# Performance work log

Measured on AMD Instinct MI355X. Metric: run time of the kernel, lower is better.

Reference implementation:

```python
import jax, jax.numpy as jnp
import numpy as np

B, S, D = 2, 2048, 2048
H, G = 32, 8           # num_heads, num_groups
HD = D // H            # head_dim = 64
GS = H // G            # group_size = 4


def setup_inputs() -> dict:
    key = jax.random.key(0)
    ks = jax.random.split(key, 11)
    s = 0.02
    return {
        "x": jax.random.normal(ks[0], (B, S, D), dtype=jnp.float32),
        "kv": jax.random.normal(ks[1], (B, S, D), dtype=jnp.float32),
        "Wq": jax.random.normal(ks[2], (D, D), dtype=jnp.float32) * s,
        "bq": jnp.zeros((D,), dtype=jnp.float32),
        "Wk": jax.random.normal(ks[3], (D, G * HD), dtype=jnp.float32) * s,
        "bk": jnp.zeros((G * HD,), dtype=jnp.float32),
        "Wv": jax.random.normal(ks[4], (D, G * HD), dtype=jnp.float32) * s,
        "bv": jnp.zeros((G * HD,), dtype=jnp.float32),
        "Wo": jax.random.normal(ks[5], (D, D), dtype=jnp.float32) * s,
        "bo": jnp.zeros((D,), dtype=jnp.float32),
        "expanding_context": 0,
    }


def reference(x, kv, Wq, bq, Wk, bk, Wv, bv, Wo, bo, expanding_context):
    # expanding_context is ignored when use_kv_cache=False (matches torch module)
    b, s, d = x.shape
    q = (x @ Wq + bq).reshape(b, s, H, HD).transpose(0, 2, 1, 3)      # [B,H,S,HD]
    k = (kv @ Wk + bk).reshape(b, s, G, HD).transpose(0, 2, 1, 3)     # [B,G,S,HD]
    v = (kv @ Wv + bv).reshape(b, s, G, HD).transpose(0, 2, 1, 3)     # [B,G,S,HD]
    # repeat_interleave KV heads to match query heads
    k = jnp.repeat(k, GS, axis=1)                                      # [B,H,S,HD]
    v = jnp.repeat(v, GS, axis=1)
    scale = 1.0 / jnp.sqrt(jnp.array(HD, dtype=x.dtype))
    scores = jnp.einsum("bhqd,bhkd->bhqk", q, k) * scale              # [B,H,S,S]
    causal = jnp.tril(jnp.ones((s, s), dtype=bool))                    # True where allowed
    scores = jnp.where(causal[None, None], scores, jnp.finfo(x.dtype).min)
    attn = jax.nn.softmax(scores, axis=-1)
    out = jnp.einsum("bhqk,bhkd->bhqd", attn, v)                      # [B,H,S,HD]
    out = out.transpose(0, 2, 1, 3).reshape(b, s, D)                  # [B,S,D]
    return out @ Wo + bo
```

## Files before the change

### kernel.cpp

```cpp
#include <hip/hip_runtime.h>
#include <hip/hip_bf16.h>
#include <stdint.h>

namespace {
constexpr int CB = 2, CS = 2048, CD = 2048, CH = 32, CG = 8, CHD = 64, CGS = 4;

typedef __bf16 bf16x8 __attribute__((ext_vector_type(8)));
typedef float f32x4 __attribute__((ext_vector_type(4)));
typedef float f32x16 __attribute__((ext_vector_type(16)));
typedef uint32_t u32x4 __attribute__((ext_vector_type(4)));

__device__ inline uint16_t f2bf(float f) {
  uint32_t u = __float_as_uint(f);
  u += 0x7fffu + ((u >> 16) & 1u);
  return (uint16_t)(u >> 16);
}

__device__ inline void gload_lds16(const void* g, void* l) {
  __builtin_amdgcn_global_load_lds(
      (const __attribute__((address_space(1))) void*)g,
      (__attribute__((address_space(3))) void*)l, 16, 0, 0);
}

__device__ inline uint32_t cvtpk_bf16(float lo, float hi) {
  uint32_t r;
  asm("v_cvt_pk_bf16_f32 %0, %1, %2" : "=v"(r) : "v"(lo), "v"(hi));
  return r;
}
__device__ inline void pl32swap(uint32_t& a, uint32_t& b) {
  asm("v_permlane32_swap_b32 %0, %1" : "+v"(a), "+v"(b));
}
}

__global__ __launch_bounds__(256) void cast_both_kernel(
    const float* __restrict__ x, const float* __restrict__ kv,
    uint16_t* __restrict__ xb, uint16_t* __restrict__ kvb, int nel) {
  int i = (blockIdx.x * 256 + threadIdx.x) * 4;
  const float* in;
  uint16_t* out;
  if (i < nel) { in = x + i; out = xb + i; }
  else         { in = kv + (i - nel); out = kvb + (i - nel); }
  const float4 v = *(const float4*)in;
  ushort4 o;
  o.x = f2bf(v.x); o.y = f2bf(v.y); o.z = f2bf(v.z); o.w = f2bf(v.w);
  *(ushort4*)out = o;
}

__global__ __launch_bounds__(256) void transpose_all_kernel(
    const float* __restrict__ Wq, const float* __restrict__ Wk,
    const float* __restrict__ Wv, const float* __restrict__ Wo,
    uint16_t* __restrict__ out) {
  __shared__ uint16_t tile[32][33];
  const int gn0 = blockIdx.x * 32;
  const int k0 = blockIdx.y * 32;
  const float* in;
  int Nr, start;
  if (gn0 < 2048)      { in = Wq; Nr = 2048; start = 0; }
  else if (gn0 < 2560) { in = Wk; Nr = 512;  start = 2048; }
  else if (gn0 < 3072) { in = Wv; Nr = 512;  start = 2560; }
  else                 { in = Wo; Nr = 2048; start = 3072; }
  const int n0 = gn0 - start;
  const int tx = threadIdx.x & 31, tg = threadIdx.x >> 5;
#pragma unroll
  for (int rr = 0; rr < 4; ++rr) {
    int k = tg * 4 + rr;
    tile[k][tx] = f2bf(in[(size_t)(k0 + k) * Nr + n0 + tx]);
  }
  __syncthreads();
#pragma unroll
  for (int rr = 0; rr < 4; ++rr) {
    int n = tg * 4 + rr;
    out[(size_t)(gn0 + n) * CD + k0 + tx] = tile[tx][n];
  }
}

__global__ __launch_bounds__(256, 2) void gemm_qkv_kernel(
    const uint16_t* __restrict__ xb, const uint16_t* __restrict__ kvb,
    const uint16_t* __restrict__ WT,
    const float* __restrict__ bq, const float* __restrict__ bk,
    const float* __restrict__ bv,
    uint16_t* __restrict__ Qb, uint16_t* __restrict__ Kb,
    uint16_t* __restrict__ VTb) {
  constexpr int BM = 128, BN = 128, BK = 32, K = 2048, NT = K / BK;
  constexpr int ASZ = BM * BK;
  constexpr int BSZ = BN * BK;
  constexpr int BUFSZ = ASZ + BSZ;
  __shared__ uint16_t smem[3 * BUFSZ];
  const int tid = threadIdx.x;
  const int w = tid >> 6, l = tid & 63;
  const int wr = w >> 1, wc = w & 1;
  const int l15 = l & 15, lq = l >> 4;

  const int gx = gridDim.x;
  int bid = blockIdx.y * gx + blockIdx.x;
  const int nwg = gx * gridDim.y;
  bid = (bid & 7) * (nwg >> 3) + (bid >> 3);
  const int m0 = (bid / gx) * BM, n0 = (bid % gx) * BN;
  const uint16_t* A = (n0 < 2048) ? xb : kvb;

  auto stage = [&](int buf, int kt) {
    uint16_t* base = smem + buf * BUFSZ;
    const int k0 = kt * BK;
#pragma unroll
    for (int i = 0; i < 2; ++i) {
      int g = i * 256 + tid;
      int row = g >> 2, slot = g & 3;
      int kq = slot ^ ((row >> 1) & 3);
      gload_lds16(A + (size_t)(m0 + row) * K + k0 + kq * 8, base + g * 8);
    }
#pragma unroll
    for (int i = 0; i < 2; ++i) {
      int g = i * 256 + tid;
      int row = g >> 2, slot = g & 3;
      int kq = slot ^ ((row >> 1) & 3);
      gload_lds16(WT + (size_t)(n0 + row) * K + k0 + kq * 8,
                  base + ASZ + g * 8);
    }
  };

  int aOff[4], bOff[4];
#pragma unroll
  for (int m = 0; m < 4; ++m) {
    int row = wr * 64 + m * 16 + l15;
    aOff[m] = (row * BK + (lq ^ ((row >> 1) & 3)) * 8) * 2;
  }
#pragma unroll
  for (int n = 0; n < 4; ++n) {
    int row = wc * 64 + n * 16 + l15;
    bOff[n] = ASZ * 2 + (row * BK + (lq ^ ((row >> 1) & 3)) * 8) * 2;
  }

  f32x4 acc[4][4] = {};

  stage(0, 0);
  stage(1, 1);

  int bt = 0, bs = 2;
  for (int t = 0; t < NT; ++t) {
    if (t < NT - 1) asm volatile("s_waitcnt vmcnt(4)" ::: "memory");
    else            asm volatile("s_waitcnt vmcnt(0)" ::: "memory");
    __builtin_amdgcn_s_barrier();
    asm volatile("" ::: "memory");

    const char* buf = (const char*)(smem + bt * BUFSZ);
    bf16x8 af[4], bfr[4];
#pragma unroll
    for (int m = 0; m < 4; ++m) af[m] = *(const bf16x8*)(buf + aOff[m]);
#pragma unroll
    for (int n = 0; n < 4; ++n) bfr[n] = *(const bf16x8*)(buf + bOff[n]);

    if (t + 2 < NT) stage(bs, t + 2);

    __builtin_amdgcn_s_setprio(1);
#pragma unroll
    for (int m = 0; m < 4; ++m)
#pragma unroll
      for (int n = 0; n < 4; ++n)
        acc[m][n] = __builtin_amdgcn_mfma_f32_16x16x32_bf16(
            af[m], bfr[n], acc[m][n], 0, 0, 0);
    __builtin_amdgcn_s_setprio(0);

    bt = bt == 2 ? 0 : bt + 1;
    bs = bs == 2 ? 0 : bs + 1;
  }

#pragma unroll
  for (int m = 0; m < 4; ++m)
#pragma unroll
    for (int n = 0; n < 4; ++n)
#pragma unroll
      for (int r = 0; r < 4; ++r) {
        int gm = m0 + wr * 64 + m * 16 + lq * 4 + r;
        int gn = n0 + wc * 64 + n * 16 + l15;
        int b = gm >> 11, s = gm & (CS - 1);
        if (n0 < 2048) {
          float v = (acc[m][n][r] + bq[gn]) * (0.125f * 1.44269504088896340736f);
          int h = gn >> 6, hd = gn & 63;
          Qb[(((size_t)(b * CH + h)) * CS + s) * CHD + hd] = f2bf(v);
        } else if (n0 < 2560) {
          int gn2 = gn - 2048;
          float v = acc[m][n][r] + bk[gn2];
          int gh = gn2 >> 6, hd = gn2 & 63;
          Kb[(((size_t)(b * CG + gh)) * CS + s) * CHD + hd] = f2bf(v);
        } else {
          int gn2 = gn - 2560;
          float v = acc[m][n][r] + bv[gn2];
          int gh = gn2 >> 6, hd = gn2 & 63;
          VTb[(((size_t)(b * CG + gh)) * CHD + hd) * CS + s] = f2bf(v);
        }
      }
}

__global__ __launch_bounds__(256, 2) void gemm_out_kernel(
    const uint16_t* __restrict__ A, const uint16_t* __restrict__ Bt,
    const float* __restrict__ bias, float* __restrict__ Cout,
    int M, int N, int Kdim) {
  constexpr int BM = 128, BN = 128, BK = 32, K = 2048, NT = K / BK;
  constexpr int ASZ = BM * BK;
  constexpr int BSZ = BN * BK;
  constexpr int BUFSZ = ASZ + BSZ;
  __shared__ uint16_t smem[3 * BUFSZ];
  const int tid = threadIdx.x;
  const int w = tid >> 6, l = tid & 63;
  const int wr = w >> 1, wc = w & 1;
  const int l15 = l & 15, lq = l >> 4;

  const int gx = gridDim.x;
  int bid = blockIdx.y * gx + blockIdx.x;
  const int nwg = gx * gridDim.y;
  bid = (bid & 7) * (nwg >> 3) + (bid >> 3);
  const int m0 = (bid / gx) * BM, n0 = (bid % gx) * BN;

  auto stage = [&](int buf, int kt) {
    uint16_t* base = smem + buf * BUFSZ;
    const int k0 = kt * BK;
#pragma unroll
    for (int i = 0; i < 2; ++i) {
      int g = i * 256 + tid;
      int row = g >> 2, slot = g & 3;
      int kq = slot ^ ((row >> 1) & 3);
      gload_lds16(A + (size_t)(m0 + row) * K + k0 + kq * 8, base + g * 8);
    }
#pragma unroll
    for (int i = 0; i < 2; ++i) {
      int g = i * 256 + tid;
      int row = g >> 2, slot = g & 3;
      int kq = slot ^ ((row >> 1) & 3);
      gload_lds16(Bt + (size_t)(n0 + row) * K + k0 + kq * 8,
                  base + ASZ + g * 8);
    }
  };

  int aOff[4], bOff[4];
#pragma unroll
  for (int m = 0; m < 4; ++m) {
    int row = wr * 64 + m * 16 + l15;
    aOff[m] = (row * BK + (lq ^ ((row >> 1) & 3)) * 8) * 2;
  }
#pragma unroll
  for (int n = 0; n < 4; ++n) {
    int row = wc * 64 + n * 16 + l15;
    bOff[n] = ASZ * 2 + (row * BK + (lq ^ ((row >> 1) & 3)) * 8) * 2;
  }

  f32x4 acc[4][4] = {};

  stage(0, 0);
  stage(1, 1);

  int bt = 0, bs = 2;
  for (int t = 0; t < NT; ++t) {
    if (t < NT - 1) asm volatile("s_waitcnt vmcnt(4)" ::: "memory");
    else            asm volatile("s_waitcnt vmcnt(0)" ::: "memory");
    __builtin_amdgcn_s_barrier();
    asm volatile("" ::: "memory");

    const char* buf = (const char*)(smem + bt * BUFSZ);
    bf16x8 af[4], bfr[4];
#pragma unroll
    for (int m = 0; m < 4; ++m) af[m] = *(const bf16x8*)(buf + aOff[m]);
#pragma unroll
    for (int n = 0; n < 4; ++n) bfr[n] = *(const bf16x8*)(buf + bOff[n]);

    if (t + 2 < NT) stage(bs, t + 2);

    __builtin_amdgcn_s_setprio(1);
#pragma unroll
    for (int m = 0; m < 4; ++m)
#pragma unroll
      for (int n = 0; n < 4; ++n)
        acc[m][n] = __builtin_amdgcn_mfma_f32_16x16x32_bf16(
            af[m], bfr[n], acc[m][n], 0, 0, 0);
    __builtin_amdgcn_s_setprio(0);

    bt = bt == 2 ? 0 : bt + 1;
    bs = bs == 2 ? 0 : bs + 1;
  }

#pragma unroll
  for (int m = 0; m < 4; ++m)
#pragma unroll
    for (int n = 0; n < 4; ++n)
#pragma unroll
      for (int r = 0; r < 4; ++r) {
        int gm = m0 + wr * 64 + m * 16 + lq * 4 + r;
        int gn = n0 + wc * 64 + n * 16 + l15;
        Cout[(size_t)gm * N + gn] = acc[m][n][r] + bias[gn];
      }
}

__global__ __launch_bounds__(256, 2) void flash_attn_kernel(
    const uint16_t* __restrict__ Q, const uint16_t* __restrict__ K,
    const uint16_t* __restrict__ VT, uint16_t* __restrict__ Aout) {
  constexpr int NQB = CS / 128;
  constexpr int KV = 128;
  __shared__ __align__(16) uint16_t Ksm[2][KV * CHD];
  __shared__ __align__(16) uint16_t Vsm[2][CHD * KV];
  const int tid = threadIdx.x, w = tid >> 6, l = tid & 63;
  const int l31 = l & 31, hi = l >> 5;
  const int x = blockIdx.x;
  const int h = blockIdx.y, b = blockIdx.z, g = h >> 2;

  const uint16_t* Qbase = Q + ((size_t)(b * CH + h)) * CS * CHD;
  const uint16_t* Kbase = K + ((size_t)(b * CG + g)) * CS * CHD;
  const uint16_t* Vbase = VT + ((size_t)(b * CG + g)) * CHD * CS;

  auto stage = [&](int buf, int kt) {
#pragma unroll
    for (int i = 0; i < 4; ++i) {
      int gK = i * 256 + tid;
      int rowK = gK >> 3, slotK = gK & 7;
      int kqK = slotK ^ (rowK & 7);
      gload_lds16(Kbase + ((size_t)kt * KV + rowK) * CHD + kqK * 8,
                  &Ksm[buf][gK * 8]);
    }
#pragma unroll
    for (int i = 0; i < 4; ++i) {
      int gV = i * 256 + tid;
      int rowV = gV >> 4, slotV = gV & 15;
      int kqV = slotV ^ (rowV & 15);
      gload_lds16(Vbase + (size_t)rowV * CS + kt * KV + kqV * 8,
                  &Vsm[buf][gV * 8]);
    }
  };

  int kOff[4][4];
#pragma unroll
  for (int c = 0; c < 4; ++c)
#pragma unroll
    for (int kc = 0; kc < 4; ++kc) {
      int row = c * 32 + l31;
      kOff[c][kc] = ((row * CHD + kc * 16 + hi * 8) * 2) ^ ((row & 7) << 4);
    }
  int vOff[2][8];
#pragma unroll
  for (int c = 0; c < 2; ++c)
#pragma unroll
    for (int ks = 0; ks < 8; ++ks) {
      int row = c * 32 + l31;
      vOff[c][ks] = ((row * KV + ks * 16 + hi * 8) * 2) ^ ((row & 15) << 4);
    }

#pragma unroll 1
  for (int job = 0; job < 2; ++job) {
    const int qb = job == 0 ? (NQB - 1 - x) : x;
    const int qrow = qb * 128 + w * 32 + l31;
    const int wbase = qb * 128 + w * 32;

    bf16x8 qf[4];
#pragma unroll
    for (int kc = 0; kc < 4; ++kc)
      qf[kc] = *(const bf16x8*)(Qbase + (size_t)qrow * CHD + kc * 16 + hi * 8);

    f32x16 o0 = {}, o1 = {};
    float mrun = -3e38f, lrun = 0.f;
    const int nt = qb + 1;

    stage(0, 0);
    asm volatile("s_waitcnt vmcnt(0)" ::: "memory");
    __syncthreads();

    for (int kt = 0; kt < nt; ++kt) {
      const int cur = kt & 1;
      if (kt + 1 < nt) stage(cur ^ 1, kt + 1);

      const char* ksmb = (const char*)Ksm[cur];
      const char* vsmb = (const char*)Vsm[cur];

      f32x16 p0 = {}, p1 = {}, p2 = {}, p3 = {};
      __builtin_amdgcn_s_setprio(1);
#pragma unroll
      for (int kc = 0; kc < 4; ++kc) {
        bf16x8 ka0 = *(const bf16x8*)(ksmb + kOff[0][kc]);
        bf16x8 ka1 = *(const bf16x8*)(ksmb + kOff[1][kc]);
        bf16x8 ka2 = *(const bf16x8*)(ksmb + kOff[2][kc]);
        bf16x8 ka3 = *(const bf16x8*)(ksmb + kOff[3][kc]);
        p0 = __builtin_amdgcn_mfma_f32_32x32x16_bf16(ka0, qf[kc], p0, 0, 0, 0);
        p1 = __builtin_amdgcn_mfma_f32_32x32x16_bf16(ka1, qf[kc], p1, 0, 0, 0);
        p2 = __builtin_amdgcn_mfma_f32_32x32x16_bf16(ka2, qf[kc], p2, 0, 0, 0);
        p3 = __builtin_amdgcn_mfma_f32_32x32x16_bf16(ka3, qf[kc], p3, 0, 0, 0);
      }
      __builtin_amdgcn_s_setprio(0);

      const bool need_mask = (kt * KV + KV - 1 > wbase);
      if (need_mask) {
#pragma unroll
        for (int r = 0; r < 16; ++r) {
          int keyb = kt * KV + (r & 3) + 8 * (r >> 2) + 4 * hi;
          if (keyb > qrow) p0[r] = -3e38f;
          if (keyb + 32 > qrow) p1[r] = -3e38f;
          if (keyb + 64 > qrow) p2[r] = -3e38f;
          if (keyb + 96 > qrow) p3[r] = -3e38f;
        }
      }
      float pmax = -3e38f;
#pragma unroll
      for (int r = 0; r < 16; ++r) {
        pmax = fmaxf(pmax, fmaxf(fmaxf(p0[r], p1[r]), fmaxf(p2[r], p3[r])));
      }
      pmax = fmaxf(pmax, __shfl_xor(pmax, 32));

      if (!__all(pmax <= mrun + 8.f)) {
        float mnew = fmaxf(mrun, pmax);
        float alpha = __builtin_amdgcn_exp2f(mrun - mnew);
#pragma unroll
        for (int r = 0; r < 16; ++r) { o0[r] *= alpha; o1[r] *= alpha; }
        lrun *= alpha;
        mrun = mnew;
      }
      float s = 0.f;
#pragma unroll
      for (int r = 0; r < 16; ++r) {
        float e0 = __builtin_amdgcn_exp2f(p0[r] - mrun);
        float e1 = __builtin_amdgcn_exp2f(p1[r] - mrun);
        float e2 = __builtin_amdgcn_exp2f(p2[r] - mrun);
        float e3 = __builtin_amdgcn_exp2f(p3[r] - mrun);
        p0[r] = e0; p1[r] = e1; p2[r] = e2; p3[r] = e3;
        s += (e0 + e1) + (e2 + e3);
      }
      s += __shfl_xor(s, 32);
      lrun += s;

      u32x4 paw[8];
#pragma unroll
      for (int k = 0; k < 8; ++k) {
        const int base = (k & 1) * 8;
        const int c = k >> 1;
        const f32x16& pc = (c == 0) ? p0 : (c == 1) ? p1 : (c == 2) ? p2 : p3;
        uint32_t c01 = cvtpk_bf16(pc[base + 0], pc[base + 1]);
        uint32_t c23 = cvtpk_bf16(pc[base + 2], pc[base + 3]);
        uint32_t c45 = cvtpk_bf16(pc[base + 4], pc[base + 5]);
        uint32_t c67 = cvtpk_bf16(pc[base + 6], pc[base + 7]);
        pl32swap(c01, c45);
        pl32swap(c23, c67);
        paw[k] = (u32x4){c01, c23, c45, c67};
      }

      __builtin_amdgcn_s_setprio(1);
#pragma unroll
      for (int ks = 0; ks < 8; ++ks) {
        bf16x8 vb0 = *(const bf16x8*)(vsmb + vOff[0][ks]);
        bf16x8 vb1 = *(const bf16x8*)(vsmb + vOff[1][ks]);
        bf16x8 pb = __builtin_bit_cast(bf16x8, paw[ks]);
        o0 = __builtin_amdgcn_mfma_f32_32x32x16_bf16(vb0, pb, o0, 0, 0, 0);
        o1 = __builtin_amdgcn_mfma_f32_32x32x16_bf16(vb1, pb, o1, 0, 0, 0);
      }
      __builtin_amdgcn_s_setprio(0);

      asm volatile("s_waitcnt vmcnt(0)" ::: "memory");
      __syncthreads();
    }

    float invl = 1.f / lrun;
    uint16_t* orow = Aout + ((size_t)b * CS + qrow) * CD + (size_t)h * CHD;
#pragma unroll
    for (int k = 0; k < 8; ++k) {
      int reg = 2 * k;
      int hd = (reg & 3) + 8 * (reg >> 2) + 4 * hi;
      *(uint32_t*)(orow + hd) = cvtpk_bf16(o0[reg] * invl, o0[reg + 1] * invl);
      *(uint32_t*)(orow + hd + 32) = cvtpk_bf16(o1[reg] * invl, o1[reg + 1] * invl);
    }
  }
}

extern "C" void kernel_launch(void* const* d_in, const int* in_sizes, int n_in,
                              void* d_out, int out_size, void* d_ws, size_t ws_size,
                              hipStream_t stream) {
  const float* x = (const float*)d_in[0];
  const float* kv = (const float*)d_in[1];
  const float* Wq = (const float*)d_in[2];
  const float* bq = (const float*)d_in[3];
  const float* Wk = (const float*)d_in[4];
  const float* bk = (const float*)d_in[5];
  const float* Wv = (const float*)d_in[6];
  const float* bv = (const float*)d_in[7];
  const float* Wo = (const float*)d_in[8];
  const float* bo = (const float*)d_in[9];
  float* out = (float*)d_out;

  char* ws = (char*)d_ws;
  uint16_t* xb = (uint16_t*)ws;   ws += (size_t)CB * CS * CD * 2;
  uint16_t* kvb = (uint16_t*)ws;  ws += (size_t)CB * CS * CD * 2;
  uint16_t* WqT = (uint16_t*)ws;  ws += (size_t)CD * CD * 2;
  uint16_t* WkT = (uint16_t*)ws;  ws += (size_t)(CG * CHD) * CD * 2;
  uint16_t* WvT = (uint16_t*)ws;  ws += (size_t)(CG * CHD) * CD * 2;
  uint16_t* WoT = (uint16_t*)ws;  ws += (size_t)CD * CD * 2;
  uint16_t* Qb = (uint16_t*)ws;   ws += (size_t)CB * CH * CS * CHD * 2;
  uint16_t* Kb = (uint16_t*)ws;   ws += (size_t)CB * CG * CS * CHD * 2;
  uint16_t* VTb = (uint16_t*)ws;  ws += (size_t)CB * CG * CHD * CS * 2;
  uint16_t* attnb = (uint16_t*)ws;
  (void)WkT; (void)WvT;

  const int NTOK = CB * CS;
  const int nel = CB * CS * CD;

  cast_both_kernel<<<2 * nel / 4 / 256, 256, 0, stream>>>(x, kv, xb, kvb, nel);
  transpose_all_kernel<<<dim3(5120 / 32, CD / 32), 256, 0, stream>>>(
      Wq, Wk, Wv, Wo, WqT);

  gemm_qkv_kernel<<<dim3(3072 / 128, NTOK / 128), 256, 0, stream>>>(
      xb, kvb, WqT, bq, bk, bv, Qb, Kb, VTb);

  flash_attn_kernel<<<dim3(CS / 256, CH, CB), 256, 0, stream>>>(Qb, Kb, VTb, attnb);

  gemm_out_kernel<<<dim3(CD / 128, NTOK / 128), 256, 0, stream>>>(
      attnb, WoT, bo, out, NTOK, CD, CD);
}
```

Before: 200.7 us.

## Pre-pack weights in MFMA fragment order and load B directly to registers

The weight transpose kernel now writes bf16 weights in a fragment-packed layout, 16-row by 32-k blocks with each lane's 8 values contiguous. Both GEMM kernels then load B operands straight from global memory into registers with one coalesced 16-byte load per lane. They stage only A through LDS, using double-buffered B registers and an unrolled even/odd loop. This removes B's LDS traffic and LDS space and is meant to cut LDS bandwidth and capacity pressure. In exchange it relies on direct global-load latency being hidden by the two-step prefetch, adds register pressure, and drops the LDS reuse of B across waves that share a column.

```diff
diff --git a/kernel.cpp b/kernel.cpp
--- a/kernel.cpp
+++ b/kernel.cpp
@@ -9,6 +9,7 @@
 typedef float f32x4 __attribute__((ext_vector_type(4)));
 typedef float f32x16 __attribute__((ext_vector_type(16)));
 typedef uint32_t u32x4 __attribute__((ext_vector_type(4)));
+typedef uint16_t u16x8 __attribute__((ext_vector_type(8)));
 
 __device__ inline uint16_t f2bf(float f) {
   uint32_t u = __float_as_uint(f);
@@ -67,25 +68,28 @@
     tile[k][tx] = f2bf(in[(size_t)(k0 + k) * Nr + n0 + tx]);
   }
   __syncthreads();
-#pragma unroll
-  for (int rr = 0; rr < 4; ++rr) {
-    int n = tg * 4 + rr;
-    out[(size_t)(gn0 + n) * CD + k0 + tx] = tile[tx][n];
+  if (threadIdx.x < 128) {
+    int n = threadIdx.x >> 2, k8 = threadIdx.x & 3;
+    u16x8 v;
+#pragma unroll
+    for (int j = 0; j < 8; ++j) v[j] = tile[k8 * 8 + j][n];
+    int n_abs = gn0 + n;
+    size_t flat = (((size_t)(n_abs >> 4) * 64 + (size_t)(k0 >> 5)) * 64 +
+                   (size_t)(k8 * 16 + (n_abs & 15))) * 8;
+    *(u16x8*)(out + flat) = v;
   }
 }
 
 __global__ __launch_bounds__(256, 2) void gemm_qkv_kernel(
     const uint16_t* __restrict__ xb, const uint16_t* __restrict__ kvb,
-    const uint16_t* __restrict__ WT,
+    const uint16_t* __restrict__ WTp,
     const float* __restrict__ bq, const float* __restrict__ bk,
     const float* __restrict__ bv,
     uint16_t* __restrict__ Qb, uint16_t* __restrict__ Kb,
     uint16_t* __restrict__ VTb) {
-  constexpr int BM = 128, BN = 128, BK = 32, K = 2048, NT = K / BK;
+  constexpr int BM = 128, BK = 32, K = 2048, NT = K / BK;
   constexpr int ASZ = BM * BK;
-  constexpr int BSZ = BN * BK;
-  constexpr int BUFSZ = ASZ + BSZ;
-  __shared__ uint16_t smem[3 * BUFSZ];
+  __shared__ uint16_t Asm[3 * ASZ];
   const int tid = threadIdx.x;
   const int w = tid >> 6, l = tid & 63;
   const int wr = w >> 1, wc = w & 1;
@@ -95,12 +99,13 @@
   int bid = blockIdx.y * gx + blockIdx.x;
   const int nwg = gx * gridDim.y;
   bid = (bid & 7) * (nwg >> 3) + (bid >> 3);
-  const int m0 = (bid / gx) * BM, n0 = (bid % gx) * BN;
+  const int m0 = (bid / gx) * BM, n0 = (bid % gx) * 128;
   const uint16_t* A = (n0 < 2048) ? xb : kvb;
-
-  auto stage = [&](int buf, int kt) {
-    uint16_t* base = smem + buf * BUFSZ;
-    const int k0 = kt * BK;
+  const int nbb = (n0 >> 4) + wc * 4;
+
+  auto stageA = [&](int buf, int t) {
+    uint16_t* base = Asm + buf * ASZ;
+    const int k0 = t * BK;
 #pragma unroll
     for (int i = 0; i < 2; ++i) {
       int g = i * 256 + tid;
@@ -108,61 +113,56 @@
       int kq = slot ^ ((row >> 1) & 3);
       gload_lds16(A + (size_t)(m0 + row) * K + k0 + kq * 8, base + g * 8);
     }
-#pragma unroll
-    for (int i = 0; i < 2; ++i) {
-      int g = i * 256 + tid;
-      int row = g >> 2, slot = g & 3;
-      int kq = slot ^ ((row >> 1) & 3);
-      gload_lds16(WT + (size_t)(n0 + row) * K + k0 + kq * 8,
-                  base + ASZ + g * 8);
-    }
   };
-
-  int aOff[4], bOff[4];
+  auto loadB = [&](bf16x8* dst, int t) {
+#pragma unroll
+    for (int n = 0; n < 4; ++n)
+      dst[n] = *(const bf16x8*)(
+          WTp + ((((size_t)(nbb + n)) * 64 + (size_t)t) << 9) + (size_t)l * 8);
+  };
+
+  int aOff[4];
 #pragma unroll
   for (int m = 0; m < 4; ++m) {
     int row = wr * 64 + m * 16 + l15;
     aOff[m] = (row * BK + (lq ^ ((row >> 1) & 3)) * 8) * 2;
   }
-#pragma unroll
-  for (int n = 0; n < 4; ++n) {
-    int row = wc * 64 + n * 16 + l15;
-    bOff[n] = ASZ * 2 + (row * BK + (lq ^ ((row >> 1) & 3)) * 8) * 2;
-  }
 
   f32x4 acc[4][4] = {};
-
-  stage(0, 0);
-  stage(1, 1);
+  bf16x8 bE[4], bO[4];
+
+  loadB(bE, 0); stageA(0, 0);
+  loadB(bO, 1); stageA(1, 1);
 
   int bt = 0, bs = 2;
-  for (int t = 0; t < NT; ++t) {
-    if (t < NT - 1) asm volatile("s_waitcnt vmcnt(4)" ::: "memory");
-    else            asm volatile("s_waitcnt vmcnt(0)" ::: "memory");
-    __builtin_amdgcn_s_barrier();
-    asm volatile("" ::: "memory");
-
-    const char* buf = (const char*)(smem + bt * BUFSZ);
-    bf16x8 af[4], bfr[4];
-#pragma unroll
-    for (int m = 0; m < 4; ++m) af[m] = *(const bf16x8*)(buf + aOff[m]);
-#pragma unroll
-    for (int n = 0; n < 4; ++n) bfr[n] = *(const bf16x8*)(buf + bOff[n]);
-
-    if (t + 2 < NT) stage(bs, t + 2);
-
-    __builtin_amdgcn_s_setprio(1);
-#pragma unroll
-    for (int m = 0; m < 4; ++m)
-#pragma unroll
-      for (int n = 0; n < 4; ++n)
-        acc[m][n] = __builtin_amdgcn_mfma_f32_16x16x32_bf16(
-            af[m], bfr[n], acc[m][n], 0, 0, 0);
-    __builtin_amdgcn_s_setprio(0);
-
-    bt = bt == 2 ? 0 : bt + 1;
-    bs = bs == 2 ? 0 : bs + 1;
-  }
+
+#define QKV_SUB(T, BREG, VM)                                                 \
+  {                                                                          \
+    asm volatile("s_waitcnt vmcnt(" #VM ")" ::: "memory");                   \
+    __builtin_amdgcn_s_barrier();                                            \
+    asm volatile("" ::: "memory");                                           \
+    const char* buf_ = (const char*)(Asm + bt * ASZ);                        \
+    bf16x8 af[4];                                                            \
+    _Pragma("unroll") for (int m = 0; m < 4; ++m)                            \
+        af[m] = *(const bf16x8*)(buf_ + aOff[m]);                            \
+    __builtin_amdgcn_s_setprio(1);                                           \
+    _Pragma("unroll") for (int m = 0; m < 4; ++m)                            \
+        _Pragma("unroll") for (int n = 0; n < 4; ++n)                        \
+            acc[m][n] = __builtin_amdgcn_mfma_f32_16x16x32_bf16(             \
+                af[m], BREG[n], acc[m][n], 0, 0, 0);                         \
+    __builtin_amdgcn_s_setprio(0);                                           \
+    if ((T) + 2 < NT) { loadB(BREG, (T) + 2); stageA(bs, (T) + 2); }         \
+    bt = bt == 2 ? 0 : bt + 1;                                               \
+    bs = bs == 2 ? 0 : bs + 1;                                               \
+  }
+
+  for (int t = 0; t < NT - 2; t += 2) {
+    QKV_SUB(t, bE, 6);
+    QKV_SUB(t + 1, bO, 6);
+  }
+  QKV_SUB(NT - 2, bE, 6);
+  QKV_SUB(NT - 1, bO, 0);
+#undef QKV_SUB
 
 #pragma unroll
   for (int m = 0; m < 4; ++m)
@@ -192,14 +192,12 @@
 }
 
 __global__ __launch_bounds__(256, 2) void gemm_out_kernel(
-    const uint16_t* __restrict__ A, const uint16_t* __restrict__ Bt,
+    const uint16_t* __restrict__ A, const uint16_t* __restrict__ Btp,
     const float* __restrict__ bias, float* __restrict__ Cout,
     int M, int N, int Kdim) {
-  constexpr int BM = 128, BN = 128, BK = 32, K = 2048, NT = K / BK;
+  constexpr int BM = 128, BK = 32, K = 2048, NT = K / BK;
   constexpr int ASZ = BM * BK;
-  constexpr int BSZ = BN * BK;
-  constexpr int BUFSZ = ASZ + BSZ;
-  __shared__ uint16_t smem[3 * BUFSZ];
+  __shared__ uint16_t Asm[3 * ASZ];
   const int tid = threadIdx.x;
   const int w = tid >> 6, l = tid & 63;
   const int wr = w >> 1, wc = w & 1;
@@ -209,11 +207,12 @@
   int bid = blockIdx.y * gx + blockIdx.x;
   const int nwg = gx * gridDim.y;
   bid = (bid & 7) * (nwg >> 3) + (bid >> 3);
-  const int m0 = (bid / gx) * BM, n0 = (bid % gx) * BN;
-
-  auto stage = [&](int buf, int kt) {
-    uint16_t* base = smem + buf * BUFSZ;
-    const int k0 = kt * BK;
+  const int m0 = (bid / gx) * BM, n0 = (bid % gx) * 128;
+  const int nbb = (n0 >> 4) + wc * 4;
+
+  auto stageA = [&](int buf, int t) {
+    uint16_t* base = Asm + buf * ASZ;
+    const int k0 = t * BK;
 #pragma unroll
     for (int i = 0; i < 2; ++i) {
       int g = i * 256 + tid;
@@ -221,61 +220,56 @@
       int kq = slot ^ ((row >> 1) & 3);
       gload_lds16(A + (size_t)(m0 + row) * K + k0 + kq * 8, base + g * 8);
     }
-#pragma unroll
-    for (int i = 0; i < 2; ++i) {
-      int g = i * 256 + tid;
-      int row = g >> 2, slot = g & 3;
-      int kq = slot ^ ((row >> 1) & 3);
-      gload_lds16(Bt + (size_t)(n0 + row) * K + k0 + kq * 8,
-                  base + ASZ + g * 8);
-    }
   };
-
-  int aOff[4], bOff[4];
+  auto loadB = [&](bf16x8* dst, int t) {
+#pragma unroll
+    for (int n = 0; n < 4; ++n)
+      dst[n] = *(const bf16x8*)(
+          Btp + ((((size_t)(nbb + n)) * 64 + (size_t)t) << 9) + (size_t)l * 8);
+  };
+
+  int aOff[4];
 #pragma unroll
   for (int m = 0; m < 4; ++m) {
     int row = wr * 64 + m * 16 + l15;
     aOff[m] = (row * BK + (lq ^ ((row >> 1) & 3)) * 8) * 2;
   }
-#pragma unroll
-  for (int n = 0; n < 4; ++n) {
-    int row = wc * 64 + n * 16 + l15;
-    bOff[n] = ASZ * 2 + (row * BK + (lq ^ ((row >> 1) & 3)) * 8) * 2;
-  }
 
   f32x4 acc[4][4] = {};
-
-  stage(0, 0);
-  stage(1, 1);
+  bf16x8 bE[4], bO[4];
+
+  loadB(bE, 0); stageA(0, 0);
+  loadB(bO, 1); stageA(1, 1);
 
   int bt = 0, bs = 2;
-  for (int t = 0; t < NT; ++t) {
-    if (t < NT - 1) asm volatile("s_waitcnt vmcnt(4)" ::: "memory");
-    else            asm volatile("s_waitcnt vmcnt(0)" ::: "memory");
-    __builtin_amdgcn_s_barrier();
-    asm volatile("" ::: "memory");
-
-    const char* buf = (const char*)(smem + bt * BUFSZ);
-    bf16x8 af[4], bfr[4];
-#pragma unroll
-    for (int m = 0; m < 4; ++m) af[m] = *(const bf16x8*)(buf + aOff[m]);
-#pragma unroll
-    for (int n = 0; n < 4; ++n) bfr[n] = *(const bf16x8*)(buf + bOff[n]);
-
-    if (t + 2 < NT) stage(bs, t + 2);
-
-    __builtin_amdgcn_s_setprio(1);
-#pragma unroll
-    for (int m = 0; m < 4; ++m)
-#pragma unroll
-      for (int n = 0; n < 4; ++n)
-        acc[m][n] = __builtin_amdgcn_mfma_f32_16x16x32_bf16(
-            af[m], bfr[n], acc[m][n], 0, 0, 0);
-    __builtin_amdgcn_s_setprio(0);
-
-    bt = bt == 2 ? 0 : bt + 1;
-    bs = bs == 2 ? 0 : bs + 1;
-  }
+
+#define OUT_SUB(T, BREG, VM)                                                 \
+  {                                                                          \
+    asm volatile("s_waitcnt vmcnt(" #VM ")" ::: "memory");                   \
+    __builtin_amdgcn_s_barrier();                                            \
+    asm volatile("" ::: "memory");                                           \
+    const char* buf_ = (const char*)(Asm + bt * ASZ);                        \
+    bf16x8 af[4];                                                            \
+    _Pragma("unroll") for (int m = 0; m < 4; ++m)                            \
+        af[m] = *(const bf16x8*)(buf_ + aOff[m]);                            \
+    __builtin_amdgcn_s_setprio(1);                                           \
+    _Pragma("unroll") for (int m = 0; m < 4; ++m)                            \
+        _Pragma("unroll") for (int n = 0; n < 4; ++n)                        \
+            acc[m][n] = __builtin_amdgcn_mfma_f32_16x16x32_bf16(             \
+                af[m], BREG[n], acc[m][n], 0, 0, 0);                         \
+    __builtin_amdgcn_s_setprio(0);                                           \
+    if ((T) + 2 < NT) { loadB(BREG, (T) + 2); stageA(bs, (T) + 2); }         \
+    bt = bt == 2 ? 0 : bt + 1;                                               \
+    bs = bs == 2 ? 0 : bs + 1;                                               \
+  }
+
+  for (int t = 0; t < NT - 2; t += 2) {
+    OUT_SUB(t, bE, 6);
+    OUT_SUB(t + 1, bO, 6);
+  }
+  OUT_SUB(NT - 2, bE, 6);
+  OUT_SUB(NT - 1, bO, 0);
+#undef OUT_SUB
 
 #pragma unroll
   for (int m = 0; m < 4; ++m)
```

After: 195.6 us. 1.03x faster.

## Pre-pack weights into MFMA fragment layout and load B directly to registers

Applied to the files above, without the earlier changes.

The weight-transpose kernel now writes weights in a fragment-packed layout, so each wave can load its B operand for an MFMA straight from global memory into registers with one contiguous 16-byte load per lane. The two GEMM kernels therefore stage only A through LDS, and BK doubles to 64, which halves the number of barrier-separated iterations. Occupancy is raised to 3 blocks per SM via launch bounds. The aim is to cut LDS traffic and per-iteration overhead. The cost is that B loads become global-latency register prefetches with only one iteration of lead time, and register pressure goes up.

```diff
diff --git a/kernel.cpp b/kernel.cpp
--- a/kernel.cpp
+++ b/kernel.cpp
@@ -9,6 +9,7 @@
 typedef float f32x4 __attribute__((ext_vector_type(4)));
 typedef float f32x16 __attribute__((ext_vector_type(16)));
 typedef uint32_t u32x4 __attribute__((ext_vector_type(4)));
+typedef uint16_t u16x8 __attribute__((ext_vector_type(8)));
 
 __device__ inline uint16_t f2bf(float f) {
   uint32_t u = __float_as_uint(f);
@@ -67,25 +68,28 @@
     tile[k][tx] = f2bf(in[(size_t)(k0 + k) * Nr + n0 + tx]);
   }
   __syncthreads();
-#pragma unroll
-  for (int rr = 0; rr < 4; ++rr) {
-    int n = tg * 4 + rr;
-    out[(size_t)(gn0 + n) * CD + k0 + tx] = tile[tx][n];
+  if (threadIdx.x < 128) {
+    int n = threadIdx.x >> 2, k8 = threadIdx.x & 3;
+    u16x8 v;
+#pragma unroll
+    for (int j = 0; j < 8; ++j) v[j] = tile[k8 * 8 + j][n];
+    int n_abs = gn0 + n;
+    size_t flat = (((size_t)(n_abs >> 4) * 64 + (size_t)(k0 >> 5)) * 64 +
+                   (size_t)(k8 * 16 + (n_abs & 15))) * 8;
+    *(u16x8*)(out + flat) = v;
   }
 }
 
-__global__ __launch_bounds__(256, 2) void gemm_qkv_kernel(
+__global__ __launch_bounds__(256, 3) void gemm_qkv_kernel(
     const uint16_t* __restrict__ xb, const uint16_t* __restrict__ kvb,
-    const uint16_t* __restrict__ WT,
+    const uint16_t* __restrict__ WTp,
     const float* __restrict__ bq, const float* __restrict__ bk,
     const float* __restrict__ bv,
     uint16_t* __restrict__ Qb, uint16_t* __restrict__ Kb,
     uint16_t* __restrict__ VTb) {
-  constexpr int BM = 128, BN = 128, BK = 32, K = 2048, NT = K / BK;
+  constexpr int BM = 128, BK = 64, K = 2048, NT = K / BK;
   constexpr int ASZ = BM * BK;
-  constexpr int BSZ = BN * BK;
-  constexpr int BUFSZ = ASZ + BSZ;
-  __shared__ uint16_t smem[3 * BUFSZ];
+  __shared__ uint16_t Asm[3 * ASZ];
   const int tid = threadIdx.x;
   const int w = tid >> 6, l = tid & 63;
   const int wr = w >> 1, wc = w & 1;
@@ -95,45 +99,46 @@
   int bid = blockIdx.y * gx + blockIdx.x;
   const int nwg = gx * gridDim.y;
   bid = (bid & 7) * (nwg >> 3) + (bid >> 3);
-  const int m0 = (bid / gx) * BM, n0 = (bid % gx) * BN;
+  const int m0 = (bid / gx) * BM, n0 = (bid % gx) * 128;
   const uint16_t* A = (n0 < 2048) ? xb : kvb;
-
-  auto stage = [&](int buf, int kt) {
-    uint16_t* base = smem + buf * BUFSZ;
-    const int k0 = kt * BK;
-#pragma unroll
-    for (int i = 0; i < 2; ++i) {
+  const int nbb = (n0 >> 4) + wc * 4;
+
+  auto stageA = [&](int buf, int t) {
+    uint16_t* base = Asm + buf * ASZ;
+    const int k0 = t * BK;
+#pragma unroll
+    for (int i = 0; i < 4; ++i) {
       int g = i * 256 + tid;
-      int row = g >> 2, slot = g & 3;
-      int kq = slot ^ ((row >> 1) & 3);
+      int row = g >> 3, slot = g & 7;
+      int kq = slot ^ (row & 7);
       gload_lds16(A + (size_t)(m0 + row) * K + k0 + kq * 8, base + g * 8);
     }
-#pragma unroll
-    for (int i = 0; i < 2; ++i) {
-      int g = i * 256 + tid;
-      int row = g >> 2, slot = g & 3;
-      int kq = slot ^ ((row >> 1) & 3);
-      gload_lds16(WT + (size_t)(n0 + row) * K + k0 + kq * 8,
-                  base + ASZ + g * 8);
-    }
   };
-
-  int aOff[4], bOff[4];
-#pragma unroll
-  for (int m = 0; m < 4; ++m) {
-    int row = wr * 64 + m * 16 + l15;
-    aOff[m] = (row * BK + (lq ^ ((row >> 1) & 3)) * 8) * 2;
-  }
-#pragma unroll
-  for (int n = 0; n < 4; ++n) {
-    int row = wc * 64 + n * 16 + l15;
-    bOff[n] = ASZ * 2 + (row * BK + (lq ^ ((row >> 1) & 3)) * 8) * 2;
-  }
+  auto loadB = [&](bf16x8 (*dst)[4], int t) {
+#pragma unroll
+    for (int kk = 0; kk < 2; ++kk)
+#pragma unroll
+      for (int n = 0; n < 4; ++n)
+        dst[kk][n] = *(const bf16x8*)(
+            WTp + ((((size_t)(nbb + n)) * 64 + (size_t)(2 * t + kk)) << 9) +
+            (size_t)l * 8);
+  };
+
+  int aOff[2][4];
+#pragma unroll
+  for (int kk = 0; kk < 2; ++kk)
+#pragma unroll
+    for (int m = 0; m < 4; ++m) {
+      int row = wr * 64 + m * 16 + l15;
+      aOff[kk][m] = (row * BK + ((kk * 4 + lq) ^ (row & 7)) * 8) * 2;
+    }
 
   f32x4 acc[4][4] = {};
-
-  stage(0, 0);
-  stage(1, 1);
+  bf16x8 brg[2][4];
+
+  loadB(brg, 0);
+  stageA(0, 0);
+  stageA(1, 1);
 
   int bt = 0, bs = 2;
   for (int t = 0; t < NT; ++t) {
@@ -142,23 +147,27 @@
     __builtin_amdgcn_s_barrier();
     asm volatile("" ::: "memory");
 
-    const char* buf = (const char*)(smem + bt * BUFSZ);
-    bf16x8 af[4], bfr[4];
-#pragma unroll
-    for (int m = 0; m < 4; ++m) af[m] = *(const bf16x8*)(buf + aOff[m]);
-#pragma unroll
-    for (int n = 0; n < 4; ++n) bfr[n] = *(const bf16x8*)(buf + bOff[n]);
-
-    if (t + 2 < NT) stage(bs, t + 2);
+    const char* buf = (const char*)(Asm + bt * ASZ);
+    bf16x8 af[2][4];
+#pragma unroll
+    for (int kk = 0; kk < 2; ++kk)
+#pragma unroll
+      for (int m = 0; m < 4; ++m)
+        af[kk][m] = *(const bf16x8*)(buf + aOff[kk][m]);
 
     __builtin_amdgcn_s_setprio(1);
 #pragma unroll
-    for (int m = 0; m < 4; ++m)
-#pragma unroll
-      for (int n = 0; n < 4; ++n)
-        acc[m][n] = __builtin_amdgcn_mfma_f32_16x16x32_bf16(
-            af[m], bfr[n], acc[m][n], 0, 0, 0);
+    for (int kk = 0; kk < 2; ++kk)
+#pragma unroll
+      for (int m = 0; m < 4; ++m)
+#pragma unroll
+        for (int n = 0; n < 4; ++n)
+          acc[m][n] = __builtin_amdgcn_mfma_f32_16x16x32_bf16(
+              af[kk][m], brg[kk][n], acc[m][n], 0, 0, 0);
     __builtin_amdgcn_s_setprio(0);
+
+    if (t + 1 < NT) loadB(brg, t + 1);
+    if (t + 2 < NT) stageA(bs, t + 2);
 
     bt = bt == 2 ? 0 : bt + 1;
     bs = bs == 2 ? 0 : bs + 1;
@@ -191,15 +200,13 @@
       }
 }
 
-__global__ __launch_bounds__(256, 2) void gemm_out_kernel(
-    const uint16_t* __restrict__ A, const uint16_t* __restrict__ Bt,
+__global__ __launch_bounds__(256, 3) void gemm_out_kernel(
+    const uint16_t* __restrict__ A, const uint16_t* __restrict__ Btp,
     const float* __restrict__ bias, float* __restrict__ Cout,
     int M, int N, int Kdim) {
-  constexpr int BM = 128, BN = 128, BK = 32, K = 2048, NT = K / BK;
+  constexpr int BM = 128, BK = 64, K = 2048, NT = K / BK;
   constexpr int ASZ = BM * BK;
-  constexpr int BSZ = BN * BK;
-  constexpr int BUFSZ = ASZ + BSZ;
-  __shared__ uint16_t smem[3 * BUFSZ];
+  __shared__ uint16_t Asm[3 * ASZ];
   const int tid = threadIdx.x;
   const int w = tid >> 6, l = tid & 63;
   const int wr = w >> 1, wc = w & 1;
@@ -209,44 +216,45 @@
   int bid = blockIdx.y * gx + blockIdx.x;
   const int nwg = gx * gridDim.y;
   bid = (bid & 7) * (nwg >> 3) + (bid >> 3);
-  const int m0 = (bid / gx) * BM, n0 = (bid % gx) * BN;
-
-  auto stage = [&](int buf, int kt) {
-    uint16_t* base = smem + buf * BUFSZ;
-    const int k0 = kt * BK;
-#pragma unroll
-    for (int i = 0; i < 2; ++i) {
+  const int m0 = (bid / gx) * BM, n0 = (bid % gx) * 128;
+  const int nbb = (n0 >> 4) + wc * 4;
+
+  auto stageA = [&](int buf, int t) {
+    uint16_t* base = Asm + buf * ASZ;
+    const int k0 = t * BK;
+#pragma unroll
+    for (int i = 0; i < 4; ++i) {
       int g = i * 256 + tid;
-      int row = g >> 2, slot = g & 3;
-      int kq = slot ^ ((row >> 1) & 3);
+      int row = g >> 3, slot = g & 7;
+      int kq = slot ^ (row & 7);
       gload_lds16(A + (size_t)(m0 + row) * K + k0 + kq * 8, base + g * 8);
     }
-#pragma unroll
-    for (int i = 0; i < 2; ++i) {
-      int g = i * 256 + tid;
-      int row = g >> 2, slot = g & 3;
-      int kq = slot ^ ((row >> 1) & 3);
-      gload_lds16(Bt + (size_t)(n0 + row) * K + k0 + kq * 8,
-                  base + ASZ + g * 8);
-    }
   };
-
-  int aOff[4], bOff[4];
-#pragma unroll
-  for (int m = 0; m < 4; ++m) {
-    int row = wr * 64 + m * 16 + l15;
-    aOff[m] = (row * BK + (lq ^ ((row >> 1) & 3)) * 8) * 2;
-  }
-#pragma unroll
-  for (int n = 0; n < 4; ++n) {
-    int row = wc * 64 + n * 16 + l15;
-    bOff[n] = ASZ * 2 + (row * BK + (lq ^ ((row >> 1) & 3)) * 8) * 2;
-  }
+  auto loadB = [&](bf16x8 (*dst)[4], int t) {
+#pragma unroll
+    for (int kk = 0; kk < 2; ++kk)
+#pragma unroll
+      for (int n = 0; n < 4; ++n)
+        dst[kk][n] = *(const bf16x8*)(
+            Btp + ((((size_t)(nbb + n)) * 64 + (size_t)(2 * t + kk)) << 9) +
+            (size_t)l * 8);
+  };
+
+  int aOff[2][4];
+#pragma unroll
+  for (int kk = 0; kk < 2; ++kk)
+#pragma unroll
+    for (int m = 0; m < 4; ++m) {
+      int row = wr * 64 + m * 16 + l15;
+      aOff[kk][m] = (row * BK + ((kk * 4 + lq) ^ (row & 7)) * 8) * 2;
+    }
 
   f32x4 acc[4][4] = {};
-
-  stage(0, 0);
-  stage(1, 1);
+  bf16x8 brg[2][4];
+
+  loadB(brg, 0);
+  stageA(0, 0);
+  stageA(1, 1);
 
   int bt = 0, bs = 2;
   for (int t = 0; t < NT; ++t) {
@@ -255,23 +263,27 @@
     __builtin_amdgcn_s_barrier();
     asm volatile("" ::: "memory");
 
-    const char* buf = (const char*)(smem + bt * BUFSZ);
-    bf16x8 af[4], bfr[4];
-#pragma unroll
-    for (int m = 0; m < 4; ++m) af[m] = *(const bf16x8*)(buf + aOff[m]);
-#pragma unroll
-    for (int n = 0; n < 4; ++n) bfr[n] = *(const bf16x8*)(buf + bOff[n]);
-
-    if (t + 2 < NT) stage(bs, t + 2);
+    const char* buf = (const char*)(Asm + bt * ASZ);
+    bf16x8 af[2][4];
+#pragma unroll
+    for (int kk = 0; kk < 2; ++kk)
+#pragma unroll
+      for (int m = 0; m < 4; ++m)
+        af[kk][m] = *(const bf16x8*)(buf + aOff[kk][m]);
 
     __builtin_amdgcn_s_setprio(1);
 #pragma unroll
-    for (int m = 0; m < 4; ++m)
-#pragma unroll
-      for (int n = 0; n < 4; ++n)
-        acc[m][n] = __builtin_amdgcn_mfma_f32_16x16x32_bf16(
-            af[m], bfr[n], acc[m][n], 0, 0, 0);
+    for (int kk = 0; kk < 2; ++kk)
+#pragma unroll
+      for (int m = 0; m < 4; ++m)
+#pragma unroll
+        for (int n = 0; n < 4; ++n)
+          acc[m][n] = __builtin_amdgcn_mfma_f32_16x16x32_bf16(
+              af[kk][m], brg[kk][n], acc[m][n], 0, 0, 0);
     __builtin_amdgcn_s_setprio(0);
+
+    if (t + 1 < NT) loadB(brg, t + 1);
+    if (t + 2 < NT) stageA(bs, t + 2);
 
     bt = bt == 2 ? 0 : bt + 1;
     bs = bs == 2 ? 0 : bs + 1;
```

After: 186.4 us, median of 3. 7.1% less time.
